# Kernel tuning notes

Measured on AMD Instinct MI355X. Metric: run time of the kernel, lower is better.

Reference implementation:

```python
import jax, jax.numpy as jnp
import numpy as np

N = 50000   # full-order mesh size
n = 10      # latent dim
MU = 32     # neighbourhood / window size
B = 8       # batch of snapshots


def setup_inputs() -> dict:
    key = jax.random.key(0)
    ks = jax.random.split(key, 6)
    x = jax.random.normal(ks[0], (B, N), jnp.float32)
    enc_w = jax.random.normal(ks[1], (n, N), jnp.float32) * 0.01  # torch Linear weight [n, N]
    enc_b = jax.random.normal(ks[2], (n,), jnp.float32) * 0.01
    decoder = jax.random.uniform(ks[3], (n, N), jnp.float32, minval=-0.01, maxval=0.01)
    bandwidth_layers = jax.random.uniform(ks[4], (n, n, N), jnp.float32, minval=-0.01, maxval=0.01)
    neighbours = jax.random.randint(ks[5], (N, MU), 0, N, jnp.int32)
    return dict(x=x, enc_w=enc_w, enc_b=enc_b, decoder=decoder,
                bandwidth_layers=bandwidth_layers, neighbours=neighbours)


def reference(x, enc_w, enc_b, decoder, bandwidth_layers, neighbours):
    mu = neighbours.shape[1]
    # encode: torch Linear -> x @ W.T + b                      [B, n]
    encoded = x @ enc_w.T + enc_b
    # bandwidths: bmm(encoded.repeat(n,1,1), bw).permute(1,0,2) -> sigmoid   [B, n, N]
    w = jax.nn.sigmoid(jnp.einsum('bk,ikp->bip', encoded, bandwidth_layers))
    # bubble window per scalar w: relu(1 - x^2/(w*mu)^2), normalized over mu  [B, n, N, mu]
    xs2 = (jnp.arange(mu, dtype=x.dtype) ** 2)  # [mu]
    win = jax.nn.relu(1.0 - xs2 / (w[..., None] * mu) ** 2)
    win = win / jnp.sum(win, axis=-1, keepdims=True)
    # gather decoder rows at each node's neighbours            [n, N, mu]
    gathered = jnp.take(decoder, neighbours, axis=1)
    # smooth_vec: sum over neighbourhood                       [B, n, N]
    smoothed = jnp.einsum('ipm,bipm->bip', gathered, win)
    # final bmm: encoded [B,1,n] @ smoothed [B,n,N] -> [B,N]
    return jnp.einsum('bi,bip->bp', encoded, smoothed)
```

## Files before the change

kernel.cpp:

```cpp
#include <hip/hip_runtime.h>
#include <hip/hip_bf16.h>

#define N_NODES 50000
#define NLAT 10
#define MU 32
#define BATCH 8
#define CHUNK 2000
#define NCHUNK 25
#define ENC_BLOCKS (BATCH * NLAT * NCHUNK)
#define TR_BLOCKS ((N_NODES + 255) / 256)
#define DT_STRIDE 16
#define NPB 32

typedef float v2f __attribute__((ext_vector_type(2)));

static __device__ __forceinline__ v2f v2_fma(v2f a, v2f b, v2f c) {
#if __has_builtin(__builtin_elementwise_fma)
    return __builtin_elementwise_fma(a, b, c);
#else
    v2f r; r[0] = fmaf(a[0], b[0], c[0]); r[1] = fmaf(a[1], b[1], c[1]); return r;
#endif
}
static __device__ __forceinline__ v2f v2_max0(v2f a) {
#if __has_builtin(__builtin_elementwise_max)
    v2f z = {0.0f, 0.0f};
    return __builtin_elementwise_max(a, z);
#else
    v2f r; r[0] = fmaxf(a[0], 0.0f); r[1] = fmaxf(a[1], 0.0f); return r;
#endif
}

__global__ __launch_bounds__(256) void encode_a_transpose(
    const float* __restrict__ x, const float* __restrict__ enc_w,
    const float* __restrict__ dec,
    float* __restrict__ partial, float* __restrict__ dec_t) {
    const int bid = blockIdx.x;
    if (bid < ENC_BLOCKS) {
        const int c  = bid % NCHUNK;
        const int bi = bid / NCHUNK;
        const int b = bi / NLAT, i = bi % NLAT;
        const float4* xr = (const float4*)(x + (size_t)b * N_NODES + c * CHUNK);
        const float4* wr = (const float4*)(enc_w + (size_t)i * N_NODES + c * CHUNK);
        float part = 0.0f;
        for (int q = threadIdx.x; q < CHUNK / 4; q += 256) {
            float4 xv = xr[q], wv = wr[q];
            part += xv.x * wv.x + xv.y * wv.y + xv.z * wv.z + xv.w * wv.w;
        }
        for (int off = 32; off; off >>= 1) part += __shfl_down(part, off, 64);
        __shared__ float s[4];
        if ((threadIdx.x & 63) == 0) s[threadIdx.x >> 6] = part;
        __syncthreads();
        if (threadIdx.x == 0) partial[bid] = (s[0] + s[1]) + (s[2] + s[3]);
    } else {
        const int p = (bid - ENC_BLOCKS) * 256 + threadIdx.x;
        if (p >= N_NODES) return;
        float v[DT_STRIDE];
        #pragma unroll
        for (int i = 0; i < NLAT; ++i) v[i] = dec[(size_t)i * N_NODES + p];
        #pragma unroll
        for (int i = NLAT; i < DT_STRIDE; ++i) v[i] = 0.0f;
        float4* dst = (float4*)(dec_t + (size_t)p * DT_STRIDE);
        #pragma unroll
        for (int q = 0; q < 4; ++q)
            dst[q] = make_float4(v[4*q], v[4*q+1], v[4*q+2], v[4*q+3]);
    }
}

__global__ __launch_bounds__(512) void nrbs_main_kernel(
    const float* __restrict__ dec_t,
    const float* __restrict__ bw,
    const int*   __restrict__ nbr,
    const float* __restrict__ partial,
    const float* __restrict__ enc_b,
    float*       __restrict__ out) {
    __shared__ float s_enc[BATCH * NLAT];
    __shared__ float s_inv[NLAT][NPB][BATCH];
    __shared__ float s_tm[NLAT][NPB];
    __shared__ int   s_nbr[NPB][MU + 1];
    const int tid   = threadIdx.x;
    const int node0 = blockIdx.x * NPB;

    if (tid < BATCH * NLAT) {
        float s = 0.0f;
        #pragma unroll
        for (int c = 0; c < NCHUNK; ++c) s += partial[tid * NCHUNK + c];
        s_enc[tid] = s + enc_b[tid % NLAT];
    }
    {
        const int j = tid;
        if (j < NPB * MU / 4) {
            const int node = j >> 3, ch = j & 7;
            int4 v = make_int4(0, 0, 0, 0);
            if (node0 + node < N_NODES)
                v = ((const int4*)(nbr + (size_t)(node0 + node) * MU))[ch];
            s_nbr[node][ch * 4 + 0] = v.x; s_nbr[node][ch * 4 + 1] = v.y;
            s_nbr[node][ch * 4 + 2] = v.z; s_nbr[node][ch * 4 + 3] = v.w;
        }
    }
    __syncthreads();

    {
        const int w    = tid >> 6;
        const int lane = tid & 63;
        const int half = lane >> 5;
        const int node = lane & 31;
        const int i    = w + 8 * half;
        const int p    = node0 + node;
        if (i < NLAT && p < N_NODES) {
            float bwv[NLAT];
            #pragma unroll
            for (int k = 0; k < NLAT; ++k)
                bwv[k] = bw[((size_t)(i * NLAT + k)) * N_NODES + p];
            float tloc = 0.0f;
            float invv[BATCH];
            #pragma unroll
            for (int b = 0; b < BATCH; ++b) {
                float z = 0.0f;
                #pragma unroll
                for (int k = 0; k < NLAT; ++k)
                    z = fmaf(s_enc[b * NLAT + k], bwv[k], z);
                const float sg = 1.0f / (1.0f + __expf(-z));
                const float t  = sg * (float)MU;
                tloc = fmaxf(tloc, t);
                invv[b] = __builtin_amdgcn_rcpf(t * t);
            }
            float4* dst = (float4*)&s_inv[i][node][0];
            dst[0] = make_float4(invv[0], invv[1], invv[2], invv[3]);
            dst[1] = make_float4(invv[4], invv[5], invv[6], invv[7]);
            s_tm[i][node] = tloc;
        }
    }
    __syncthreads();

    const int node  = tid >> 4;
    const int islot = tid & 15;
    const int p     = node0 + node;
    const bool act  = (islot < NLAT) && (p < N_NODES);

    v2f inv2[4], asum[4], ssum[4];
    #pragma unroll
    for (int b2 = 0; b2 < 4; ++b2) {
        inv2[b2] = (v2f){0.0f, 0.0f};
        asum[b2] = (v2f){0.0f, 0.0f};
        ssum[b2] = (v2f){0.0f, 0.0f};
    }
    int mcap = 0;
    if (act) {
        const float4* iv = (const float4*)&s_inv[islot][node][0];
        const float4 a = iv[0], c = iv[1];
        inv2[0] = (v2f){a.x, a.y}; inv2[1] = (v2f){a.z, a.w};
        inv2[2] = (v2f){c.x, c.y}; inv2[3] = (v2f){c.z, c.w};
        mcap = min(MU, (int)s_tm[islot][node] + 1);
    }

    for (int m = 0; m < mcap; ++m) {
        const int idx = s_nbr[node][m];
        const float g = dec_t[(size_t)idx * DT_STRIDE + islot];
        const float m2 = (float)(m * m);
        const v2f nm2 = {-m2, -m2}, one = {1.0f, 1.0f}, gg = {g, g};
        #pragma unroll
        for (int b2 = 0; b2 < 4; ++b2) {
            const v2f win = v2_max0(v2_fma(nm2, inv2[b2], one));
            ssum[b2] += win;
            asum[b2] = v2_fma(gg, win, asum[b2]);
        }
    }

    float r[BATCH];
    #pragma unroll
    for (int b2 = 0; b2 < 4; ++b2)
        #pragma unroll
        for (int h = 0; h < 2; ++h) {
            const int b = 2 * b2 + h;
            r[b] = act ? s_enc[b * NLAT + islot] * asum[b2][h] *
                         __builtin_amdgcn_rcpf(ssum[b2][h])
                       : 0.0f;
        }
    #pragma unroll
    for (int mask = 1; mask < 16; mask <<= 1)
        #pragma unroll
        for (int b = 0; b < BATCH; ++b)
            r[b] += __shfl_xor(r[b], mask, 16);

    if (islot == 0 && p < N_NODES) {
        #pragma unroll
        for (int b = 0; b < BATCH; ++b)
            out[(size_t)b * N_NODES + p] = r[b];
    }
}

extern "C" void kernel_launch(void* const* d_in, const int* in_sizes, int n_in,
                              void* d_out, int out_size, void* d_ws, size_t ws_size,
                              hipStream_t stream) {
    const float* x       = (const float*)d_in[0];
    const float* enc_w   = (const float*)d_in[1];
    const float* enc_b   = (const float*)d_in[2];
    const float* decoder = (const float*)d_in[3];
    const float* bwl     = (const float*)d_in[4];
    const int*   nbr     = (const int*)d_in[5];
    float* out = (float*)d_out;

    float* partial = (float*)((char*)d_ws + 1024);
    float* dec_t   = (float*)((char*)d_ws + 65536);

    encode_a_transpose<<<ENC_BLOCKS + TR_BLOCKS, 256, 0, stream>>>(
        x, enc_w, decoder, partial, dec_t);

    const int blocks = (N_NODES + NPB - 1) / NPB;
    nrbs_main_kernel<<<blocks, 512, 0, stream>>>(
        dec_t, bwl, nbr, partial, enc_b, out);
}
```

Measured before the change: 107.6 us.

## Process two latent dims per thread and 64 nodes per block in main kernel

Doubles nodes per block to 64 and reassigns threads so each handles a pair of latent dimensions, loading both decoder values with one 8-byte gather per neighbour. The per-(i,node) loop bound becomes one per-node max shared across all latent dims via a shared atomicMax. The shuffle reduction shrinks to 8 lanes, and each lane writes one batch output instead of one lane writing all eight. This halves idle lanes (10 of 16 slots before versus 5 of 8) and cuts redundant index loads, at the cost of more registers per thread and loop trip counts that can no longer be trimmed per latent dimension.

```diff
diff --git a/kernel.cpp b/kernel.cpp
--- a/kernel.cpp
+++ b/kernel.cpp
@@ -10,7 +10,7 @@
 #define ENC_BLOCKS (BATCH * NLAT * NCHUNK)
 #define TR_BLOCKS ((N_NODES + 255) / 256)
 #define DT_STRIDE 16
-#define NPB 32
+#define NPB 64
 
 typedef float v2f __attribute__((ext_vector_type(2)));
 
@@ -75,7 +75,7 @@
     float*       __restrict__ out) {
     __shared__ float s_enc[BATCH * NLAT];
     __shared__ float s_inv[NLAT][NPB][BATCH];
-    __shared__ float s_tm[NLAT][NPB];
+    __shared__ int   s_tm[NPB];
     __shared__ int   s_nbr[NPB][MU + 1];
     const int tid   = threadIdx.x;
     const int node0 = blockIdx.x * NPB;
@@ -86,83 +86,90 @@
         for (int c = 0; c < NCHUNK; ++c) s += partial[tid * NCHUNK + c];
         s_enc[tid] = s + enc_b[tid % NLAT];
     }
+    if (tid < NPB) s_tm[tid] = 0;
     {
-        const int j = tid;
-        if (j < NPB * MU / 4) {
-            const int node = j >> 3, ch = j & 7;
-            int4 v = make_int4(0, 0, 0, 0);
-            if (node0 + node < N_NODES)
-                v = ((const int4*)(nbr + (size_t)(node0 + node) * MU))[ch];
-            s_nbr[node][ch * 4 + 0] = v.x; s_nbr[node][ch * 4 + 1] = v.y;
-            s_nbr[node][ch * 4 + 2] = v.z; s_nbr[node][ch * 4 + 3] = v.w;
-        }
+        const int node = tid >> 3, ch = tid & 7;
+        int4 v = make_int4(0, 0, 0, 0);
+        if (node0 + node < N_NODES)
+            v = ((const int4*)(nbr + (size_t)(node0 + node) * MU))[ch];
+        s_nbr[node][ch * 4 + 0] = v.x; s_nbr[node][ch * 4 + 1] = v.y;
+        s_nbr[node][ch * 4 + 2] = v.z; s_nbr[node][ch * 4 + 3] = v.w;
     }
     __syncthreads();
 
     {
-        const int w    = tid >> 6;
+        const int g    = tid >> 6;
         const int lane = tid & 63;
-        const int half = lane >> 5;
-        const int node = lane & 31;
-        const int i    = w + 8 * half;
-        const int p    = node0 + node;
-        if (i < NLAT && p < N_NODES) {
-            float bwv[NLAT];
-            #pragma unroll
-            for (int k = 0; k < NLAT; ++k)
-                bwv[k] = bw[((size_t)(i * NLAT + k)) * N_NODES + p];
+        const int p    = node0 + lane;
+        if (p < N_NODES) {
             float tloc = 0.0f;
-            float invv[BATCH];
-            #pragma unroll
-            for (int b = 0; b < BATCH; ++b) {
-                float z = 0.0f;
+            for (int i = g; i < NLAT; i += 8) {
+                float bwv[NLAT];
                 #pragma unroll
                 for (int k = 0; k < NLAT; ++k)
-                    z = fmaf(s_enc[b * NLAT + k], bwv[k], z);
-                const float sg = 1.0f / (1.0f + __expf(-z));
-                const float t  = sg * (float)MU;
-                tloc = fmaxf(tloc, t);
-                invv[b] = __builtin_amdgcn_rcpf(t * t);
+                    bwv[k] = bw[((size_t)(i * NLAT + k)) * N_NODES + p];
+                float invv[BATCH];
+                #pragma unroll
+                for (int b = 0; b < BATCH; ++b) {
+                    float z = 0.0f;
+                    #pragma unroll
+                    for (int k = 0; k < NLAT; ++k)
+                        z = fmaf(s_enc[b * NLAT + k], bwv[k], z);
+                    const float sg = 1.0f / (1.0f + __expf(-z));
+                    const float t  = sg * (float)MU;
+                    tloc = fmaxf(tloc, t);
+                    invv[b] = __builtin_amdgcn_rcpf(t * t);
+                }
+                float4* dst = (float4*)&s_inv[i][lane][0];
+                dst[0] = make_float4(invv[0], invv[1], invv[2], invv[3]);
+                dst[1] = make_float4(invv[4], invv[5], invv[6], invv[7]);
             }
-            float4* dst = (float4*)&s_inv[i][node][0];
-            dst[0] = make_float4(invv[0], invv[1], invv[2], invv[3]);
-            dst[1] = make_float4(invv[4], invv[5], invv[6], invv[7]);
-            s_tm[i][node] = tloc;
+            atomicMax(&s_tm[lane], __float_as_int(tloc));
         }
     }
     __syncthreads();
 
-    const int node  = tid >> 4;
-    const int islot = tid & 15;
+    const int node  = tid >> 3;
+    const int ipair = tid & 7;
     const int p     = node0 + node;
-    const bool act  = (islot < NLAT) && (p < N_NODES);
-
-    v2f inv2[4], asum[4], ssum[4];
+    const int i0    = 2 * ipair;
+    const bool act  = (ipair < 5) && (p < N_NODES);
+
+    v2f inv2[2][4], asum[2][4], ssum[2][4];
     #pragma unroll
-    for (int b2 = 0; b2 < 4; ++b2) {
-        inv2[b2] = (v2f){0.0f, 0.0f};
-        asum[b2] = (v2f){0.0f, 0.0f};
-        ssum[b2] = (v2f){0.0f, 0.0f};
-    }
+    for (int ii = 0; ii < 2; ++ii)
+        #pragma unroll
+        for (int b2 = 0; b2 < 4; ++b2) {
+            inv2[ii][b2] = (v2f){0.0f, 0.0f};
+            asum[ii][b2] = (v2f){0.0f, 0.0f};
+            ssum[ii][b2] = (v2f){0.0f, 0.0f};
+        }
     int mcap = 0;
     if (act) {
-        const float4* iv = (const float4*)&s_inv[islot][node][0];
-        const float4 a = iv[0], c = iv[1];
-        inv2[0] = (v2f){a.x, a.y}; inv2[1] = (v2f){a.z, a.w};
-        inv2[2] = (v2f){c.x, c.y}; inv2[3] = (v2f){c.z, c.w};
-        mcap = min(MU, (int)s_tm[islot][node] + 1);
+        #pragma unroll
+        for (int ii = 0; ii < 2; ++ii) {
+            const float4* iv = (const float4*)&s_inv[i0 + ii][node][0];
+            const float4 a = iv[0], c = iv[1];
+            inv2[ii][0] = (v2f){a.x, a.y}; inv2[ii][1] = (v2f){a.z, a.w};
+            inv2[ii][2] = (v2f){c.x, c.y}; inv2[ii][3] = (v2f){c.z, c.w};
+        }
+        mcap = min(MU, (int)__int_as_float(s_tm[node]) + 1);
     }
 
     for (int m = 0; m < mcap; ++m) {
         const int idx = s_nbr[node][m];
-        const float g = dec_t[(size_t)idx * DT_STRIDE + islot];
+        const v2f g2 = *(const v2f*)(dec_t + (size_t)idx * DT_STRIDE + i0);
         const float m2 = (float)(m * m);
-        const v2f nm2 = {-m2, -m2}, one = {1.0f, 1.0f}, gg = {g, g};
-        #pragma unroll
-        for (int b2 = 0; b2 < 4; ++b2) {
-            const v2f win = v2_max0(v2_fma(nm2, inv2[b2], one));
-            ssum[b2] += win;
-            asum[b2] = v2_fma(gg, win, asum[b2]);
+        const v2f nm2 = {-m2, -m2}, one = {1.0f, 1.0f};
+        #pragma unroll
+        for (int ii = 0; ii < 2; ++ii) {
+            const v2f gg = {g2[ii], g2[ii]};
+            #pragma unroll
+            for (int b2 = 0; b2 < 4; ++b2) {
+                const v2f win = v2_max0(v2_fma(nm2, inv2[ii][b2], one));
+                ssum[ii][b2] += win;
+                asum[ii][b2] = v2_fma(gg, win, asum[ii][b2]);
+            }
         }
     }
 
@@ -172,21 +179,20 @@
         #pragma unroll
         for (int h = 0; h < 2; ++h) {
             const int b = 2 * b2 + h;
-            r[b] = act ? s_enc[b * NLAT + islot] * asum[b2][h] *
-                         __builtin_amdgcn_rcpf(ssum[b2][h])
+            r[b] = act ? s_enc[b * NLAT + i0]     * asum[0][b2][h] *
+                             __builtin_amdgcn_rcpf(ssum[0][b2][h]) +
+                         s_enc[b * NLAT + i0 + 1] * asum[1][b2][h] *
+                             __builtin_amdgcn_rcpf(ssum[1][b2][h])
                        : 0.0f;
         }
     #pragma unroll
-    for (int mask = 1; mask < 16; mask <<= 1)
+    for (int mask = 1; mask < 8; mask <<= 1)
         #pragma unroll
         for (int b = 0; b < BATCH; ++b)
-            r[b] += __shfl_xor(r[b], mask, 16);
-
-    if (islot == 0 && p < N_NODES) {
-        #pragma unroll
-        for (int b = 0; b < BATCH; ++b)
-            out[(size_t)b * N_NODES + p] = r[b];
-    }
+            r[b] += __shfl_xor(r[b], mask, 8);
+
+    if (p < N_NODES)
+        out[(size_t)ipair * N_NODES + p] = r[ipair];
 }
 
 extern "C" void kernel_launch(void* const* d_in, const int* in_sizes, int n_in,
```

Result: no change. 107.3 us (-0.2%).
